# Kernel optimization log

Measured on AMD Instinct MI355X. Metric: run time of the kernel, lower is better.

## Reference

```python
import jax, jax.numpy as jnp
import numpy as np

B, S, D = 2, 1024, 2048
H, KVH, HD = 16, 4, 128
E, K, F = 64, 8, 768
EPS = 1e-6
ROPE_THETA = 1e6


def _rmsnorm(x, w):
    xf = x.astype(jnp.float32)
    n = xf * jax.lax.rsqrt(jnp.mean(xf * xf, axis=-1, keepdims=True) + EPS)
    return n.astype(x.dtype) * w


def _rotate_half(x):
    x1, x2 = jnp.split(x, 2, axis=-1)
    return jnp.concatenate([-x2, x1], axis=-1)


def setup_inputs() -> dict:
    key = jax.random.key(0)
    ks = jax.random.split(key, 12)
    std = 0.02
    x = jax.random.normal(ks[0], (B, S, D), jnp.float32)
    # real RoPE tables (HF style: duplicated half-freqs)
    inv_freq = 1.0 / (ROPE_THETA ** (jnp.arange(0, HD, 2, dtype=jnp.float32) / HD))
    freqs = jnp.arange(S, dtype=jnp.float32)[:, None] * inv_freq[None, :]
    emb = jnp.concatenate([freqs, freqs], axis=-1)  # [S, HD]
    cos = jnp.broadcast_to(jnp.cos(emb)[None], (B, S, HD))
    sin = jnp.broadcast_to(jnp.sin(emb)[None], (B, S, HD))
    return dict(
        x=x, cos=cos, sin=sin,
        ln1_w=jnp.ones((D,), jnp.float32),
        wq=jax.random.normal(ks[1], (D, H * HD), jnp.float32) * std,
        wk=jax.random.normal(ks[2], (D, KVH * HD), jnp.float32) * std,
        wv=jax.random.normal(ks[3], (D, KVH * HD), jnp.float32) * std,
        wo=jax.random.normal(ks[4], (H * HD, D), jnp.float32) * std,
        qn_w=jnp.ones((HD,), jnp.float32),
        kn_w=jnp.ones((HD,), jnp.float32),
        ln2_w=jnp.ones((D,), jnp.float32),
        router_w=jax.random.normal(ks[5], (D, E), jnp.float32) * std,
        w_gate=jax.random.normal(ks[6], (E, D, F), jnp.float32) * std,
        w_up=jax.random.normal(ks[7], (E, D, F), jnp.float32) * std,
        w_down=jax.random.normal(ks[8], (E, F, D), jnp.float32) * std,
    )


def reference(x, cos, sin, ln1_w, wq, wk, wv, wo, qn_w, kn_w, ln2_w,
              router_w, w_gate, w_up, w_down):
    # ---- attention sub-block (pre-norm) ----
    h = _rmsnorm(x, ln1_w)
    q = (h @ wq).reshape(B, S, H, HD)
    k = (h @ wk).reshape(B, S, KVH, HD)
    v = (h @ wv).reshape(B, S, KVH, HD)
    q = _rmsnorm(q, qn_w)  # QK-norm before RoPE
    k = _rmsnorm(k, kn_w)
    q = q.transpose(0, 2, 1, 3)  # [B,H,S,HD]
    k = k.transpose(0, 2, 1, 3)
    v = v.transpose(0, 2, 1, 3)
    c, sn = cos[:, None], sin[:, None]  # [B,1,S,HD]
    q = q * c + _rotate_half(q) * sn
    k = k * c + _rotate_half(k) * sn
    rep = H // KVH
    k = jnp.repeat(k, rep, axis=1)  # GQA repeat_interleave
    v = jnp.repeat(v, rep, axis=1)
    scores = jnp.einsum('bhqd,bhkd->bhqk', q, k) / np.float32(np.sqrt(HD))
    causal = jnp.tril(jnp.ones((S, S), bool))
    scores = jnp.where(causal, scores, jnp.float32(-1e30))
    attn = jax.nn.softmax(scores, axis=-1)
    o = jnp.einsum('bhqk,bhkd->bhqd', attn, v)
    o = o.transpose(0, 2, 1, 3).reshape(B, S, H * HD)
    x = x + o @ wo

    # ---- MoE sub-block (token-choice top-k routing) ----
    T = B * S
    ht = _rmsnorm(x, ln2_w).reshape(T, D)
    logits = ht.astype(jnp.float32) @ router_w
    probs = jax.nn.softmax(logits, axis=-1)  # [T,E]
    topv, topi = jax.lax.top_k(probs, K)
    topv = topv / jnp.sum(topv, axis=-1, keepdims=True)  # norm_topk_prob

    flat_e = topi.reshape(-1)                       # [T*K] expert id per assignment
    flat_t = jnp.repeat(jnp.arange(T), K)           # token id per assignment
    order = jnp.argsort(flat_e)                     # group assignments by expert
    tok = flat_t[order]
    xs = ht[tok]                                    # [T*K, D] dispatched tokens
    group_sizes = jax.ops.segment_sum(
        jnp.ones_like(flat_e, jnp.int32), flat_e, num_segments=E)

    g = jax.lax.ragged_dot(xs, w_gate, group_sizes)         # grouped GEMM
    u = jax.lax.ragged_dot(xs, w_up, group_sizes)
    y = jax.lax.ragged_dot(jax.nn.silu(g) * u, w_down, group_sizes)

    wts = topv.reshape(-1)[order]
    moe = jnp.zeros((T, D), x.dtype).at[tok].add(y * wts[:, None])
    return x + moe.reshape(B, S, D)
```

## Files before the change

### kernel.cpp

```cpp
#include <hip/hip_runtime.h>
#include <math.h>

#define NB     2
#define SEQ    1024
#define TOKS   2048
#define DMODEL 2048
#define NH     16
#define NKV    4
#define HDIM   128
#define NEXP   64
#define TOPK   8
#define FFD    768

__global__ __launch_bounds__(256) void rmsnorm2048_kernel(const float* __restrict__ x,
                                                          const float* __restrict__ w,
                                                          float* __restrict__ out) {
    int t = blockIdx.x;
    const float* xr = x + (size_t)t * DMODEL;
    float* orow = out + (size_t)t * DMODEL;
    int tid = threadIdx.x;
    float4 a = ((const float4*)xr)[tid * 2];
    float4 b = ((const float4*)xr)[tid * 2 + 1];
    float ss = a.x*a.x + a.y*a.y + a.z*a.z + a.w*a.w
             + b.x*b.x + b.y*b.y + b.z*b.z + b.w*b.w;
    __shared__ float red[256];
    red[tid] = ss;
    __syncthreads();
    for (int s = 128; s > 0; s >>= 1) {
        if (tid < s) red[tid] += red[tid + s];
        __syncthreads();
    }
    float rs = rsqrtf(red[0] * (1.0f / DMODEL) + 1e-6f);
    float4 w0 = ((const float4*)w)[tid * 2];
    float4 w1 = ((const float4*)w)[tid * 2 + 1];
    float4 o0, o1;
    o0.x = a.x * rs * w0.x; o0.y = a.y * rs * w0.y; o0.z = a.z * rs * w0.z; o0.w = a.w * rs * w0.w;
    o1.x = b.x * rs * w1.x; o1.y = b.y * rs * w1.y; o1.z = b.z * rs * w1.z; o1.w = b.w * rs * w1.w;
    ((float4*)orow)[tid * 2] = o0;
    ((float4*)orow)[tid * 2 + 1] = o1;
}

__global__ __launch_bounds__(256) void gemm128_kernel(const float* __restrict__ A,
                                                      const float* __restrict__ Bm,
                                                      const float* __restrict__ resid,
                                                      float* __restrict__ C,
                                                      int M, int N, int K) {
    __shared__ float As[16][132];
    __shared__ float Bs[16][132];
    int tid = threadIdx.x;
    int bm = blockIdx.y * 128, bn = blockIdx.x * 128;
    int tx = tid & 15, ty = tid >> 4;
    float acc[8][8];
#pragma unroll
    for (int i = 0; i < 8; ++i)
#pragma unroll
        for (int j = 0; j < 8; ++j) acc[i][j] = 0.f;

    int arow = tid >> 1, acol = (tid & 1) * 8;
    int brow = tid >> 4, bcol = (tid & 15) * 8;
    const float* Aptr = A + (size_t)(bm + arow) * K + acol;
    const float* Bptr = Bm + (size_t)brow * N + bn + bcol;

    for (int k0 = 0; k0 < K; k0 += 16) {
        float4 a0 = *(const float4*)(Aptr + k0);
        float4 a1 = *(const float4*)(Aptr + k0 + 4);
        As[acol + 0][arow] = a0.x; As[acol + 1][arow] = a0.y;
        As[acol + 2][arow] = a0.z; As[acol + 3][arow] = a0.w;
        As[acol + 4][arow] = a1.x; As[acol + 5][arow] = a1.y;
        As[acol + 6][arow] = a1.z; As[acol + 7][arow] = a1.w;
        const float* bp = Bptr + (size_t)k0 * N;
        *(float4*)&Bs[brow][bcol]     = *(const float4*)bp;
        *(float4*)&Bs[brow][bcol + 4] = *(const float4*)(bp + 4);
        __syncthreads();
#pragma unroll
        for (int k = 0; k < 16; ++k) {
            float a[8], b[8];
#pragma unroll
            for (int i = 0; i < 8; ++i) a[i] = As[k][ty * 8 + i];
#pragma unroll
            for (int j = 0; j < 8; ++j) b[j] = Bs[k][tx * 8 + j];
#pragma unroll
            for (int i = 0; i < 8; ++i)
#pragma unroll
                for (int j = 0; j < 8; ++j) acc[i][j] += a[i] * b[j];
        }
        __syncthreads();
    }
#pragma unroll
    for (int i = 0; i < 8; ++i) {
        size_t rowoff = (size_t)(bm + ty * 8 + i) * N + bn + tx * 8;
        float4 c0 = make_float4(acc[i][0], acc[i][1], acc[i][2], acc[i][3]);
        float4 c1 = make_float4(acc[i][4], acc[i][5], acc[i][6], acc[i][7]);
        if (resid) {
            float4 r0 = *(const float4*)(resid + rowoff);
            float4 r1 = *(const float4*)(resid + rowoff + 4);
            c0.x += r0.x; c0.y += r0.y; c0.z += r0.z; c0.w += r0.w;
            c1.x += r1.x; c1.y += r1.y; c1.z += r1.z; c1.w += r1.w;
        }
        *(float4*)(C + rowoff) = c0;
        *(float4*)(C + rowoff + 4) = c1;
    }
}

__global__ __launch_bounds__(128) void qknorm_rope_kernel(float* __restrict__ q, float* __restrict__ kbuf,
                                                          const float* __restrict__ qn_w,
                                                          const float* __restrict__ kn_w,
                                                          const float* __restrict__ cosb,
                                                          const float* __restrict__ sinb) {
    int t = blockIdx.x;
    int head = blockIdx.y;
    int d = threadIdx.x;
    float* buf; const float* w;
    if (head < NH) { buf = q + ((size_t)t * NH + head) * HDIM; w = qn_w; }
    else           { buf = kbuf + ((size_t)t * NKV + (head - NH)) * HDIM; w = kn_w; }
    float v = buf[d];
    __shared__ float red[128];
    __shared__ float nb[128];
    red[d] = v * v;
    __syncthreads();
    for (int s = 64; s > 0; s >>= 1) { if (d < s) red[d] += red[d + s]; __syncthreads(); }
    float rs = rsqrtf(red[0] * (1.0f / HDIM) + 1e-6f);
    float n = v * rs * w[d];
    nb[d] = n;
    __syncthreads();
    float rh = (d < 64) ? -nb[d + 64] : nb[d - 64];
    float c  = cosb[(size_t)t * HDIM + d];
    float s2 = sinb[(size_t)t * HDIM + d];
    buf[d] = n * c + rh * s2;
}

__global__ __launch_bounds__(256) void attn_kernel(const float* __restrict__ q,
                                                   const float* __restrict__ kb,
                                                   const float* __restrict__ vb,
                                                   float* __restrict__ o) {
    int bh = blockIdx.x;
    int b = bh >> 4, hh = bh & 15;
    int kvh = hh >> 2;
    int qt = blockIdx.y;
    int m0 = qt * 32;
    int tid = threadIdx.x;
    __shared__ float Qs[32][132];
    __shared__ float Ks[32][132];
    __shared__ float Vs[32][132];
    __shared__ float Ss[32][33];
    __shared__ float rowm[32], rowl[32], rowa[32];
    const float scale = 0.08838834764831845f;

    int lr = tid >> 3, lc = (tid & 7) * 16;
    {
        const float* src = q + (((size_t)(b * SEQ + m0 + lr)) * NH + hh) * HDIM + lc;
#pragma unroll
        for (int p = 0; p < 4; ++p) {
            float4 v4 = *(const float4*)(src + p * 4);
            Qs[lr][lc + p * 4 + 0] = v4.x * scale;
            Qs[lr][lc + p * 4 + 1] = v4.y * scale;
            Qs[lr][lc + p * 4 + 2] = v4.z * scale;
            Qs[lr][lc + p * 4 + 3] = v4.w * scale;
        }
    }
    if (tid < 32) { rowm[tid] = -1e30f; rowl[tid] = 0.f; }
    float oacc[16];
#pragma unroll
    for (int j = 0; j < 16; ++j) oacc[j] = 0.f;
    int mrow = tid & 31, dbase = (tid >> 5) * 16;
    int mi = tid >> 3, kbase = (tid & 7) * 4;
    __syncthreads();

    for (int kt = 0; kt <= qt; ++kt) {
        int k0 = kt * 32;
        {
            const float* ksrc = kb + (((size_t)(b * SEQ + k0 + lr)) * NKV + kvh) * HDIM + lc;
            const float* vsrc = vb + (((size_t)(b * SEQ + k0 + lr)) * NKV + kvh) * HDIM + lc;
#pragma unroll
            for (int p = 0; p < 4; ++p) {
                *(float4*)&Ks[lr][lc + p * 4] = *(const float4*)(ksrc + p * 4);
                *(float4*)&Vs[lr][lc + p * 4] = *(const float4*)(vsrc + p * 4);
            }
        }
        __syncthreads();
        float sc[4] = {0.f, 0.f, 0.f, 0.f};
#pragma unroll 8
        for (int d4 = 0; d4 < 32; ++d4) {
            float4 qv = *(const float4*)&Qs[mi][d4 * 4];
#pragma unroll
            for (int i = 0; i < 4; ++i) {
                float4 kv = *(const float4*)&Ks[kbase + i][d4 * 4];
                sc[i] += qv.x * kv.x + qv.y * kv.y + qv.z * kv.z + qv.w * kv.w;
            }
        }
#pragma unroll
        for (int i = 0; i < 4; ++i) {
            int kg = k0 + kbase + i;
            Ss[mi][kbase + i] = (kg <= m0 + mi) ? sc[i] : -1e30f;
        }
        __syncthreads();
        if (tid < 32) {
            float mold = rowm[tid];
            float tm = mold;
            for (int j = 0; j < 32; ++j) tm = fmaxf(tm, Ss[tid][j]);
            float al = __expf(mold - tm);
            float sum = 0.f;
            for (int j = 0; j < 32; ++j) {
                float p = __expf(Ss[tid][j] - tm);
                Ss[tid][j] = p;
                sum += p;
            }
            rowa[tid] = al; rowm[tid] = tm;
            rowl[tid] = rowl[tid] * al + sum;
        }
        __syncthreads();
        float al = rowa[mrow];
#pragma unroll
        for (int j = 0; j < 16; ++j) oacc[j] *= al;
        for (int kk = 0; kk < 32; ++kk) {
            float p = Ss[mrow][kk];
            const float* vrow = &Vs[kk][dbase];
#pragma unroll
            for (int j = 0; j < 16; ++j) oacc[j] += p * vrow[j];
        }
        __syncthreads();
    }
    float linv = 1.0f / rowl[mrow];
    float* dst = o + ((size_t)(b * SEQ + m0 + mrow)) * DMODEL + hh * HDIM + dbase;
#pragma unroll
    for (int p = 0; p < 4; ++p) {
        float4 v4 = make_float4(oacc[p * 4 + 0] * linv, oacc[p * 4 + 1] * linv,
                                oacc[p * 4 + 2] * linv, oacc[p * 4 + 3] * linv);
        *(float4*)(dst + p * 4) = v4;
    }
}

__global__ __launch_bounds__(64) void router_kernel(const float* __restrict__ ht,
                                                    const float* __restrict__ rw,
                                                    float* __restrict__ logits) {
    int t = blockIdx.x; int e = threadIdx.x;
    const float* hrow = ht + (size_t)t * DMODEL;
    float acc = 0.f;
    for (int d = 0; d < DMODEL; ++d) acc = fmaf(hrow[d], rw[(size_t)d * NEXP + e], acc);
    logits[(size_t)t * NEXP + e] = acc;
}

__global__ __launch_bounds__(64) void topk_kernel(const float* __restrict__ logits,
                                                  float* __restrict__ topw,
                                                  int* __restrict__ topi) {
    int t = blockIdx.x; int lane = threadIdx.x;
    float v = logits[(size_t)t * NEXP + lane];
    float mx = v;
#pragma unroll
    for (int off = 32; off; off >>= 1) mx = fmaxf(mx, __shfl_xor(mx, off));
    float myv = v;
    float sel_v[TOPK]; int sel_i[TOPK];
#pragma unroll
    for (int it = 0; it < TOPK; ++it) {
        float bv = myv; int bi = lane;
#pragma unroll
        for (int off = 32; off; off >>= 1) {
            float ov = __shfl_xor(bv, off);
            int oi = __shfl_xor(bi, off);
            if (ov > bv || (ov == bv && oi < bi)) { bv = ov; bi = oi; }
        }
        sel_v[it] = bv; sel_i[it] = bi;
        if (lane == bi) myv = -3e38f;
    }
    float sum = 0.f;
#pragma unroll
    for (int it = 0; it < TOPK; ++it) sum += __expf(sel_v[it] - mx);
    if (lane == 0) {
#pragma unroll
        for (int it = 0; it < TOPK; ++it) {
            topw[(size_t)t * TOPK + it] = __expf(sel_v[it] - mx) / sum;
            topi[(size_t)t * TOPK + it] = sel_i[it];
        }
    }
}

__global__ void zero_small_kernel(int* cnt, int* pos) {
    int i = threadIdx.x;
    if (i < NEXP) { cnt[i] = 0; pos[i] = 0; }
}
__global__ void hist_kernel(const int* __restrict__ topi, int* __restrict__ cnt) {
    int i = blockIdx.x * 256 + threadIdx.x;
    if (i < TOKS * TOPK) atomicAdd(&cnt[topi[i]], 1);
}
__global__ void scan_kernel(const int* __restrict__ cnt, int* __restrict__ eoff) {
    if (threadIdx.x == 0) {
        int a = 0;
        for (int e = 0; e < NEXP; ++e) { eoff[e] = a; a += cnt[e]; }
    }
}
__global__ void scatter_kernel(const int* __restrict__ topi, const float* __restrict__ topw,
                               const int* __restrict__ eoff, int* __restrict__ pos,
                               int* __restrict__ tokl, float* __restrict__ wtl) {
    int i = blockIdx.x * 256 + threadIdx.x;
    if (i >= TOKS * TOPK) return;
    int e = topi[i];
    int slot = atomicAdd(&pos[e], 1);
    int idx = eoff[e] + slot;
    tokl[idx] = i >> 3;
    wtl[idx] = topw[i];
}

__global__ __launch_bounds__(256) void moe_gateup_kernel(const float* __restrict__ ht,
                                                         const float* __restrict__ wg,
                                                         const float* __restrict__ wu,
                                                         const int* __restrict__ tokl,
                                                         const float* __restrict__ wtl,
                                                         const int* __restrict__ eoff,
                                                         const int* __restrict__ ecnt,
                                                         float* __restrict__ act) {
    int e = blockIdx.x, ft = blockIdx.y, mt = blockIdx.z;
    int ne = ecnt[e];
    int r0 = mt * 64;
    if (r0 >= ne) return;
    int base = eoff[e];
    int tid = threadIdx.x;
    __shared__ float As[16][68];
    __shared__ float Gs[16][64];
    __shared__ float Us[16][64];
    int arow = tid >> 2, acol = (tid & 3) * 4;
    int grow = r0 + arow;
    const float* asrc = (grow < ne) ? (ht + (size_t)tokl[base + grow] * DMODEL) : nullptr;
    int wrow = tid >> 4, wcol = (tid & 15) * 4;
    const float* wgp = wg + (size_t)e * DMODEL * FFD + (size_t)ft * 64;
    const float* wup = wu + (size_t)e * DMODEL * FFD + (size_t)ft * 64;
    int tx = tid & 15, ty = tid >> 4;
    float aG[4][4], aU[4][4];
#pragma unroll
    for (int i = 0; i < 4; ++i)
#pragma unroll
        for (int j = 0; j < 4; ++j) { aG[i][j] = 0.f; aU[i][j] = 0.f; }

    for (int k0 = 0; k0 < DMODEL; k0 += 16) {
        float4 av = asrc ? *(const float4*)(asrc + k0 + acol) : make_float4(0.f, 0.f, 0.f, 0.f);
        As[acol + 0][arow] = av.x; As[acol + 1][arow] = av.y;
        As[acol + 2][arow] = av.z; As[acol + 3][arow] = av.w;
        *(float4*)&Gs[wrow][wcol] = *(const float4*)(wgp + (size_t)(k0 + wrow) * FFD + wcol);
        *(float4*)&Us[wrow][wcol] = *(const float4*)(wup + (size_t)(k0 + wrow) * FFD + wcol);
        __syncthreads();
#pragma unroll
        for (int k = 0; k < 16; ++k) {
            float a[4], g[4], u[4];
#pragma unroll
            for (int i = 0; i < 4; ++i) a[i] = As[k][ty * 4 + i];
#pragma unroll
            for (int j = 0; j < 4; ++j) { g[j] = Gs[k][tx * 4 + j]; u[j] = Us[k][tx * 4 + j]; }
#pragma unroll
            for (int i = 0; i < 4; ++i)
#pragma unroll
                for (int j = 0; j < 4; ++j) {
                    aG[i][j] += a[i] * g[j];
                    aU[i][j] += a[i] * u[j];
                }
        }
        __syncthreads();
    }
#pragma unroll
    for (int i = 0; i < 4; ++i) {
        int gr = r0 + ty * 4 + i;
        if (gr < ne) {
            float wt = wtl[base + gr];
            float* dst = act + (size_t)(base + gr) * FFD + ft * 64 + tx * 4;
#pragma unroll
            for (int j = 0; j < 4; ++j) {
                float g = aG[i][j];
                float sg = g / (1.f + __expf(-g));
                dst[j] = sg * aU[i][j] * wt;
            }
        }
    }
}

__global__ __launch_bounds__(256) void moe_down_kernel(const float* __restrict__ act,
                                                       const float* __restrict__ wd,
                                                       const int* __restrict__ tokl,
                                                       const int* __restrict__ eoff,
                                                       const int* __restrict__ ecnt,
                                                       float* __restrict__ out) {
    int e = blockIdx.x, dt = blockIdx.y, mt = blockIdx.z;
    int ne = ecnt[e];
    int r0 = mt * 64;
    if (r0 >= ne) return;
    int base = eoff[e];
    int tid = threadIdx.x;
    __shared__ float As[16][68];
    __shared__ float Ws[16][64];
    int arow = tid >> 2, acol = (tid & 3) * 4;
    int grow = r0 + arow;
    const float* asrc = (grow < ne) ? (act + (size_t)(base + grow) * FFD) : nullptr;
    int wrow = tid >> 4, wcol = (tid & 15) * 4;
    const float* wdp = wd + (size_t)e * FFD * DMODEL + (size_t)dt * 64;
    int tx = tid & 15, ty = tid >> 4;
    float acc[4][4];
#pragma unroll
    for (int i = 0; i < 4; ++i)
#pragma unroll
        for (int j = 0; j < 4; ++j) acc[i][j] = 0.f;

    for (int k0 = 0; k0 < FFD; k0 += 16) {
        float4 av = asrc ? *(const float4*)(asrc + k0 + acol) : make_float4(0.f, 0.f, 0.f, 0.f);
        As[acol + 0][arow] = av.x; As[acol + 1][arow] = av.y;
        As[acol + 2][arow] = av.z; As[acol + 3][arow] = av.w;
        *(float4*)&Ws[wrow][wcol] = *(const float4*)(wdp + (size_t)(k0 + wrow) * DMODEL + wcol);
        __syncthreads();
#pragma unroll
        for (int k = 0; k < 16; ++k) {
            float a[4], b[4];
#pragma unroll
            for (int i = 0; i < 4; ++i) a[i] = As[k][ty * 4 + i];
#pragma unroll
            for (int j = 0; j < 4; ++j) b[j] = Ws[k][tx * 4 + j];
#pragma unroll
            for (int i = 0; i < 4; ++i)
#pragma unroll
                for (int j = 0; j < 4; ++j) acc[i][j] += a[i] * b[j];
        }
        __syncthreads();
    }
#pragma unroll
    for (int i = 0; i < 4; ++i) {
        int gr = r0 + ty * 4 + i;
        if (gr < ne) {
            int tok = tokl[base + gr];
            float* dst = out + (size_t)tok * DMODEL + dt * 64 + tx * 4;
#pragma unroll
            for (int j = 0; j < 4; ++j) atomicAdd(dst + j, acc[i][j]);
        }
    }
}

extern "C" void kernel_launch(void* const* d_in, const int* in_sizes, int n_in,
                              void* d_out, int out_size, void* d_ws, size_t ws_size,
                              hipStream_t stream) {
    const float* x    = (const float*)d_in[0];
    const float* cosb = (const float*)d_in[1];
    const float* sinb = (const float*)d_in[2];
    const float* ln1  = (const float*)d_in[3];
    const float* wq   = (const float*)d_in[4];
    const float* wk   = (const float*)d_in[5];
    const float* wv   = (const float*)d_in[6];
    const float* wo   = (const float*)d_in[7];
    const float* qnw  = (const float*)d_in[8];
    const float* knw  = (const float*)d_in[9];
    const float* ln2  = (const float*)d_in[10];
    const float* rw   = (const float*)d_in[11];
    const float* wg   = (const float*)d_in[12];
    const float* wu   = (const float*)d_in[13];
    const float* wd   = (const float*)d_in[14];
    float* out = (float*)d_out;

    float* ws     = (float*)d_ws;
    float* h      = ws;
    float* qb     = h + 4194304;
    float* kbuf   = qb + 4194304;
    float* vbuf   = kbuf + 1048576;
    float* act    = vbuf + 1048576;
    float* logits = act + 12582912;
    float* topw   = logits + 131072;
    float* wtl    = topw + 16384;
    int* topi     = (int*)(wtl + 16384);
    int* tokl     = topi + 16384;
    int* cnt      = tokl + 16384;
    int* eoff     = cnt + 64;
    int* pos      = eoff + 64;
    float* attn_o = h;
    float* ht     = qb;

    rmsnorm2048_kernel<<<TOKS, 256, 0, stream>>>(x, ln1, h);
    gemm128_kernel<<<dim3(16, 16), 256, 0, stream>>>(h, wq, nullptr, qb, TOKS, 2048, DMODEL);
    gemm128_kernel<<<dim3(4, 16), 256, 0, stream>>>(h, wk, nullptr, kbuf, TOKS, 512, DMODEL);
    gemm128_kernel<<<dim3(4, 16), 256, 0, stream>>>(h, wv, nullptr, vbuf, TOKS, 512, DMODEL);
    qknorm_rope_kernel<<<dim3(TOKS, NH + NKV), 128, 0, stream>>>(qb, kbuf, qnw, knw, cosb, sinb);
    attn_kernel<<<dim3(NB * NH, SEQ / 32), 256, 0, stream>>>(qb, kbuf, vbuf, attn_o);
    gemm128_kernel<<<dim3(16, 16), 256, 0, stream>>>(attn_o, wo, x, out, TOKS, 2048, DMODEL);
    rmsnorm2048_kernel<<<TOKS, 256, 0, stream>>>(out, ln2, ht);
    router_kernel<<<TOKS, 64, 0, stream>>>(ht, rw, logits);
    topk_kernel<<<TOKS, 64, 0, stream>>>(logits, topw, topi);
    zero_small_kernel<<<1, 64, 0, stream>>>(cnt, pos);
    hist_kernel<<<64, 256, 0, stream>>>(topi, cnt);
    scan_kernel<<<1, 1, 0, stream>>>(cnt, eoff);
    scatter_kernel<<<64, 256, 0, stream>>>(topi, topw, eoff, pos, tokl, wtl);
    moe_gateup_kernel<<<dim3(NEXP, FFD / 64, 32), 256, 0, stream>>>(ht, wg, wu, tokl, wtl, eoff, cnt, act);
    moe_down_kernel<<<dim3(NEXP, DMODEL / 64, 32), 256, 0, stream>>>(act, wd, tokl, eoff, cnt, out);
}
```

Before: 5.000 ms.

## Use split-bf16 MFMA for MoE grouped GEMMs with precomputed hi/lo activations

Replaces the scalar FP32 MoE gate/up and down GEMMs with MFMA bf16 kernels. Each operand is split into bf16 hi and lo parts and multiplied with three MFMAs to approximate FP32 accuracy. The second rmsnorm now also writes bf16 hi/lo copies of the normalized activations, and the gate/up kernel stores the activation as hi/lo bf16. Weights are still read as fp32 and split on the fly, using an XOR-swizzled LDS layout. The grid order is changed so that tiles of the same expert are adjacent. The cost is extra conversion work and a small loss of precision from dropping the lo*lo term.

```diff
diff --git a/kernel.cpp b/kernel.cpp
--- a/kernel.cpp
+++ b/kernel.cpp
@@ -12,9 +12,24 @@
 #define TOPK   8
 #define FFD    768
 
+typedef __attribute__((ext_vector_type(8))) short bf16x8;
+typedef __attribute__((ext_vector_type(4))) float f32x4;
+
+__device__ __forceinline__ void split2(float a, float b, unsigned int& hp, unsigned int& lp) {
+    unsigned int h, l;
+    asm("v_cvt_pk_bf16_f32 %0, %1, %2" : "=v"(h) : "v"(a), "v"(b));
+    float hf0 = __uint_as_float(h << 16);
+    float hf1 = __uint_as_float(h & 0xffff0000u);
+    float l0 = a - hf0, l1 = b - hf1;
+    asm("v_cvt_pk_bf16_f32 %0, %1, %2" : "=v"(l) : "v"(l0), "v"(l1));
+    hp = h; lp = l;
+}
+
 __global__ __launch_bounds__(256) void rmsnorm2048_kernel(const float* __restrict__ x,
                                                           const float* __restrict__ w,
-                                                          float* __restrict__ out) {
+                                                          float* __restrict__ out,
+                                                          unsigned short* __restrict__ hi,
+                                                          unsigned short* __restrict__ lo) {
     int t = blockIdx.x;
     const float* xr = x + (size_t)t * DMODEL;
     float* orow = out + (size_t)t * DMODEL;
@@ -38,6 +53,16 @@
     o1.x = b.x * rs * w1.x; o1.y = b.y * rs * w1.y; o1.z = b.z * rs * w1.z; o1.w = b.w * rs * w1.w;
     ((float4*)orow)[tid * 2] = o0;
     ((float4*)orow)[tid * 2 + 1] = o1;
+    if (hi) {
+        unsigned int h0, l0_, h1, l1_, h2, l2_, h3, l3_;
+        split2(o0.x, o0.y, h0, l0_);
+        split2(o0.z, o0.w, h1, l1_);
+        split2(o1.x, o1.y, h2, l2_);
+        split2(o1.z, o1.w, h3, l3_);
+        size_t off = (size_t)t * DMODEL + (size_t)tid * 8;
+        *(uint4*)(hi + off) = make_uint4(h0, h1, h2, h3);
+        *(uint4*)(lo + off) = make_uint4(l0_, l1_, l2_, l3_);
+    }
 }
 
 __global__ __launch_bounds__(256) void gemm128_kernel(const float* __restrict__ A,
@@ -300,132 +325,228 @@
     wtl[idx] = topw[i];
 }
 
-__global__ __launch_bounds__(256) void moe_gateup_kernel(const float* __restrict__ ht,
-                                                         const float* __restrict__ wg,
-                                                         const float* __restrict__ wu,
-                                                         const int* __restrict__ tokl,
-                                                         const float* __restrict__ wtl,
-                                                         const int* __restrict__ eoff,
-                                                         const int* __restrict__ ecnt,
-                                                         float* __restrict__ act) {
-    int e = blockIdx.x, ft = blockIdx.y, mt = blockIdx.z;
+#define LROW 40
+__device__ __forceinline__ int lds_off(int row, int kc) {
+    return row * LROW + (((kc ^ (row >> 3)) & 3) << 3);
+}
+
+__global__ __launch_bounds__(256) void moe_gateup_mfma(
+        const unsigned short* __restrict__ hthi, const unsigned short* __restrict__ htlo,
+        const float* __restrict__ wg, const float* __restrict__ wu,
+        const int* __restrict__ tokl, const float* __restrict__ wtl,
+        const int* __restrict__ eoff, const int* __restrict__ ecnt,
+        unsigned short* __restrict__ acthi, unsigned short* __restrict__ actlo) {
+    int mt = blockIdx.x, ft = blockIdx.y, e = blockIdx.z;
     int ne = ecnt[e];
     int r0 = mt * 64;
     if (r0 >= ne) return;
     int base = eoff[e];
     int tid = threadIdx.x;
-    __shared__ float As[16][68];
-    __shared__ float Gs[16][64];
-    __shared__ float Us[16][64];
-    int arow = tid >> 2, acol = (tid & 3) * 4;
-    int grow = r0 + arow;
-    const float* asrc = (grow < ne) ? (ht + (size_t)tokl[base + grow] * DMODEL) : nullptr;
-    int wrow = tid >> 4, wcol = (tid & 15) * 4;
-    const float* wgp = wg + (size_t)e * DMODEL * FFD + (size_t)ft * 64;
-    const float* wup = wu + (size_t)e * DMODEL * FFD + (size_t)ft * 64;
-    int tx = tid & 15, ty = tid >> 4;
-    float aG[4][4], aU[4][4];
-#pragma unroll
-    for (int i = 0; i < 4; ++i)
-#pragma unroll
-        for (int j = 0; j < 4; ++j) { aG[i][j] = 0.f; aU[i][j] = 0.f; }
-
-    for (int k0 = 0; k0 < DMODEL; k0 += 16) {
-        float4 av = asrc ? *(const float4*)(asrc + k0 + acol) : make_float4(0.f, 0.f, 0.f, 0.f);
-        As[acol + 0][arow] = av.x; As[acol + 1][arow] = av.y;
-        As[acol + 2][arow] = av.z; As[acol + 3][arow] = av.w;
-        *(float4*)&Gs[wrow][wcol] = *(const float4*)(wgp + (size_t)(k0 + wrow) * FFD + wcol);
-        *(float4*)&Us[wrow][wcol] = *(const float4*)(wup + (size_t)(k0 + wrow) * FFD + wcol);
-        __syncthreads();
-#pragma unroll
-        for (int k = 0; k < 16; ++k) {
-            float a[4], g[4], u[4];
-#pragma unroll
-            for (int i = 0; i < 4; ++i) a[i] = As[k][ty * 4 + i];
-#pragma unroll
-            for (int j = 0; j < 4; ++j) { g[j] = Gs[k][tx * 4 + j]; u[j] = Us[k][tx * 4 + j]; }
-#pragma unroll
-            for (int i = 0; i < 4; ++i)
-#pragma unroll
-                for (int j = 0; j < 4; ++j) {
-                    aG[i][j] += a[i] * g[j];
-                    aU[i][j] += a[i] * u[j];
-                }
-        }
-        __syncthreads();
-    }
-#pragma unroll
-    for (int i = 0; i < 4; ++i) {
-        int gr = r0 + ty * 4 + i;
-        if (gr < ne) {
-            float wt = wtl[base + gr];
-            float* dst = act + (size_t)(base + gr) * FFD + ft * 64 + tx * 4;
-#pragma unroll
-            for (int j = 0; j < 4; ++j) {
-                float g = aG[i][j];
-                float sg = g / (1.f + __expf(-g));
-                dst[j] = sg * aU[i][j] * wt;
+
+    __shared__ __align__(16) unsigned short Ah[64 * LROW], Al[64 * LROW];
+    __shared__ __align__(16) unsigned short Gh[64 * LROW], Gl[64 * LROW];
+    __shared__ __align__(16) unsigned short Uh[64 * LROW], Ul[64 * LROW];
+
+    int arow = tid >> 2, akc = tid & 3;
+    const unsigned short* ahsrc = nullptr;
+    const unsigned short* alsrc = nullptr;
+    if (r0 + arow < ne) {
+        size_t o = (size_t)tokl[base + r0 + arow] * DMODEL + akc * 8;
+        ahsrc = hthi + o;
+        alsrc = htlo + o;
+    }
+    int bn = tid & 63, bkc = tid >> 6;
+    const float* wgp = wg + (size_t)e * DMODEL * FFD + (size_t)ft * 64 + bn;
+    const float* wup = wu + (size_t)e * DMODEL * FFD + (size_t)ft * 64 + bn;
+
+    int lane = tid & 63, wave = tid >> 6;
+    int wr = wave >> 1, wc = wave & 1;
+    int lrow = lane & 15, lkc = lane >> 4;
+
+    f32x4 z4 = {0.f, 0.f, 0.f, 0.f};
+    f32x4 accG[2][2], accU[2][2];
+#pragma unroll
+    for (int m = 0; m < 2; ++m)
+#pragma unroll
+        for (int n = 0; n < 2; ++n) { accG[m][n] = z4; accU[m][n] = z4; }
+
+    int aoff[2], boff[2];
+#pragma unroll
+    for (int m = 0; m < 2; ++m) aoff[m] = lds_off(wr * 32 + m * 16 + lrow, lkc);
+#pragma unroll
+    for (int n = 0; n < 2; ++n) boff[n] = lds_off(wc * 32 + n * 16 + lrow, lkc);
+    int awoff = lds_off(arow, akc);
+    int bwoff = lds_off(bn, bkc);
+
+    const bf16x8 zero8 = {0, 0, 0, 0, 0, 0, 0, 0};
+
+    for (int k0 = 0; k0 < DMODEL; k0 += 32) {
+        bf16x8 avh = ahsrc ? *(const bf16x8*)(ahsrc + k0) : zero8;
+        bf16x8 avl = alsrc ? *(const bf16x8*)(alsrc + k0) : zero8;
+        float gv[8], uv[8];
+#pragma unroll
+        for (int j = 0; j < 8; ++j) {
+            size_t ro = (size_t)(k0 + bkc * 8 + j) * FFD;
+            gv[j] = wgp[ro];
+            uv[j] = wup[ro];
+        }
+        unsigned int ghp[4], glp[4], uhp[4], ulp[4];
+#pragma unroll
+        for (int p = 0; p < 4; ++p) {
+            split2(gv[2 * p], gv[2 * p + 1], ghp[p], glp[p]);
+            split2(uv[2 * p], uv[2 * p + 1], uhp[p], ulp[p]);
+        }
+        __syncthreads();
+        *(bf16x8*)(Ah + awoff) = avh;
+        *(bf16x8*)(Al + awoff) = avl;
+        *(uint4*)(Gh + bwoff) = make_uint4(ghp[0], ghp[1], ghp[2], ghp[3]);
+        *(uint4*)(Gl + bwoff) = make_uint4(glp[0], glp[1], glp[2], glp[3]);
+        *(uint4*)(Uh + bwoff) = make_uint4(uhp[0], uhp[1], uhp[2], uhp[3]);
+        *(uint4*)(Ul + bwoff) = make_uint4(ulp[0], ulp[1], ulp[2], ulp[3]);
+        __syncthreads();
+
+        bf16x8 a_h[2], a_l[2];
+#pragma unroll
+        for (int m = 0; m < 2; ++m) {
+            a_h[m] = *(const bf16x8*)(Ah + aoff[m]);
+            a_l[m] = *(const bf16x8*)(Al + aoff[m]);
+        }
+#pragma unroll
+        for (int n = 0; n < 2; ++n) {
+            bf16x8 g_h = *(const bf16x8*)(Gh + boff[n]);
+            bf16x8 g_l = *(const bf16x8*)(Gl + boff[n]);
+            bf16x8 u_h = *(const bf16x8*)(Uh + boff[n]);
+            bf16x8 u_l = *(const bf16x8*)(Ul + boff[n]);
+#pragma unroll
+            for (int m = 0; m < 2; ++m) {
+                accG[m][n] = __builtin_amdgcn_mfma_f32_16x16x32_bf16(a_h[m], g_h, accG[m][n], 0, 0, 0);
+                accG[m][n] = __builtin_amdgcn_mfma_f32_16x16x32_bf16(a_l[m], g_h, accG[m][n], 0, 0, 0);
+                accG[m][n] = __builtin_amdgcn_mfma_f32_16x16x32_bf16(a_h[m], g_l, accG[m][n], 0, 0, 0);
+                accU[m][n] = __builtin_amdgcn_mfma_f32_16x16x32_bf16(a_h[m], u_h, accU[m][n], 0, 0, 0);
+                accU[m][n] = __builtin_amdgcn_mfma_f32_16x16x32_bf16(a_l[m], u_h, accU[m][n], 0, 0, 0);
+                accU[m][n] = __builtin_amdgcn_mfma_f32_16x16x32_bf16(a_h[m], u_l, accU[m][n], 0, 0, 0);
             }
         }
     }
-}
-
-__global__ __launch_bounds__(256) void moe_down_kernel(const float* __restrict__ act,
-                                                       const float* __restrict__ wd,
-                                                       const int* __restrict__ tokl,
-                                                       const int* __restrict__ eoff,
-                                                       const int* __restrict__ ecnt,
-                                                       float* __restrict__ out) {
-    int e = blockIdx.x, dt = blockIdx.y, mt = blockIdx.z;
+
+    int crow4 = (lane >> 4) * 4;
+#pragma unroll
+    for (int m = 0; m < 2; ++m)
+#pragma unroll
+        for (int r = 0; r < 4; ++r) {
+            int gr = r0 + wr * 32 + m * 16 + crow4 + r;
+            if (gr < ne) {
+                float wt = wtl[base + gr];
+                size_t rowoff = (size_t)(base + gr) * FFD + ft * 64 + wc * 32 + lrow;
+                float g0 = accG[m][0][r], g1 = accG[m][1][r];
+                float u0 = accU[m][0][r], u1 = accU[m][1][r];
+                float x0 = g0 / (1.f + __expf(-g0)) * u0 * wt;
+                float x1 = g1 / (1.f + __expf(-g1)) * u1 * wt;
+                unsigned int hp, lp;
+                split2(x0, x1, hp, lp);
+                acthi[rowoff]      = (unsigned short)(hp & 0xffffu);
+                acthi[rowoff + 16] = (unsigned short)(hp >> 16);
+                actlo[rowoff]      = (unsigned short)(lp & 0xffffu);
+                actlo[rowoff + 16] = (unsigned short)(lp >> 16);
+            }
+        }
+}
+
+__global__ __launch_bounds__(256) void moe_down_mfma(
+        const unsigned short* __restrict__ acthi, const unsigned short* __restrict__ actlo,
+        const float* __restrict__ wd,
+        const int* __restrict__ tokl, const int* __restrict__ eoff, const int* __restrict__ ecnt,
+        float* __restrict__ out) {
+    int mt = blockIdx.x, dt = blockIdx.y, e = blockIdx.z;
     int ne = ecnt[e];
     int r0 = mt * 64;
     if (r0 >= ne) return;
     int base = eoff[e];
     int tid = threadIdx.x;
-    __shared__ float As[16][68];
-    __shared__ float Ws[16][64];
-    int arow = tid >> 2, acol = (tid & 3) * 4;
-    int grow = r0 + arow;
-    const float* asrc = (grow < ne) ? (act + (size_t)(base + grow) * FFD) : nullptr;
-    int wrow = tid >> 4, wcol = (tid & 15) * 4;
-    const float* wdp = wd + (size_t)e * FFD * DMODEL + (size_t)dt * 64;
-    int tx = tid & 15, ty = tid >> 4;
-    float acc[4][4];
-#pragma unroll
-    for (int i = 0; i < 4; ++i)
-#pragma unroll
-        for (int j = 0; j < 4; ++j) acc[i][j] = 0.f;
-
-    for (int k0 = 0; k0 < FFD; k0 += 16) {
-        float4 av = asrc ? *(const float4*)(asrc + k0 + acol) : make_float4(0.f, 0.f, 0.f, 0.f);
-        As[acol + 0][arow] = av.x; As[acol + 1][arow] = av.y;
-        As[acol + 2][arow] = av.z; As[acol + 3][arow] = av.w;
-        *(float4*)&Ws[wrow][wcol] = *(const float4*)(wdp + (size_t)(k0 + wrow) * DMODEL + wcol);
-        __syncthreads();
-#pragma unroll
-        for (int k = 0; k < 16; ++k) {
-            float a[4], b[4];
-#pragma unroll
-            for (int i = 0; i < 4; ++i) a[i] = As[k][ty * 4 + i];
-#pragma unroll
-            for (int j = 0; j < 4; ++j) b[j] = Ws[k][tx * 4 + j];
-#pragma unroll
-            for (int i = 0; i < 4; ++i)
-#pragma unroll
-                for (int j = 0; j < 4; ++j) acc[i][j] += a[i] * b[j];
-        }
-        __syncthreads();
-    }
-#pragma unroll
-    for (int i = 0; i < 4; ++i) {
-        int gr = r0 + ty * 4 + i;
-        if (gr < ne) {
-            int tok = tokl[base + gr];
-            float* dst = out + (size_t)tok * DMODEL + dt * 64 + tx * 4;
-#pragma unroll
-            for (int j = 0; j < 4; ++j) atomicAdd(dst + j, acc[i][j]);
-        }
-    }
+
+    __shared__ __align__(16) unsigned short Ah[64 * LROW], Al[64 * LROW];
+    __shared__ __align__(16) unsigned short Wh[64 * LROW], Wl[64 * LROW];
+
+    int arow = tid >> 2, akc = tid & 3;
+    const unsigned short* ahsrc = nullptr;
+    const unsigned short* alsrc = nullptr;
+    if (r0 + arow < ne) {
+        size_t o = (size_t)(base + r0 + arow) * FFD + akc * 8;
+        ahsrc = acthi + o;
+        alsrc = actlo + o;
+    }
+    int bn = tid & 63, bkc = tid >> 6;
+    const float* wdp = wd + (size_t)e * FFD * DMODEL + (size_t)dt * 64 + bn;
+
+    int lane = tid & 63, wave = tid >> 6;
+    int wr = wave >> 1, wc = wave & 1;
+    int lrow = lane & 15, lkc = lane >> 4;
+
+    f32x4 z4 = {0.f, 0.f, 0.f, 0.f};
+    f32x4 acc[2][2];
+#pragma unroll
+    for (int m = 0; m < 2; ++m)
+#pragma unroll
+        for (int n = 0; n < 2; ++n) acc[m][n] = z4;
+
+    int aoff[2], boff[2];
+#pragma unroll
+    for (int m = 0; m < 2; ++m) aoff[m] = lds_off(wr * 32 + m * 16 + lrow, lkc);
+#pragma unroll
+    for (int n = 0; n < 2; ++n) boff[n] = lds_off(wc * 32 + n * 16 + lrow, lkc);
+    int awoff = lds_off(arow, akc);
+    int bwoff = lds_off(bn, bkc);
+
+    const bf16x8 zero8 = {0, 0, 0, 0, 0, 0, 0, 0};
+
+    for (int k0 = 0; k0 < FFD; k0 += 32) {
+        bf16x8 avh = ahsrc ? *(const bf16x8*)(ahsrc + k0) : zero8;
+        bf16x8 avl = alsrc ? *(const bf16x8*)(alsrc + k0) : zero8;
+        float wv[8];
+#pragma unroll
+        for (int j = 0; j < 8; ++j) wv[j] = wdp[(size_t)(k0 + bkc * 8 + j) * DMODEL];
+        unsigned int whp[4], wlp[4];
+#pragma unroll
+        for (int p = 0; p < 4; ++p) split2(wv[2 * p], wv[2 * p + 1], whp[p], wlp[p]);
+        __syncthreads();
+        *(bf16x8*)(Ah + awoff) = avh;
+        *(bf16x8*)(Al + awoff) = avl;
+        *(uint4*)(Wh + bwoff) = make_uint4(whp[0], whp[1], whp[2], whp[3]);
+        *(uint4*)(Wl + bwoff) = make_uint4(wlp[0], wlp[1], wlp[2], wlp[3]);
+        __syncthreads();
+
+        bf16x8 a_h[2], a_l[2];
+#pragma unroll
+        for (int m = 0; m < 2; ++m) {
+            a_h[m] = *(const bf16x8*)(Ah + aoff[m]);
+            a_l[m] = *(const bf16x8*)(Al + aoff[m]);
+        }
+#pragma unroll
+        for (int n = 0; n < 2; ++n) {
+            bf16x8 w_h = *(const bf16x8*)(Wh + boff[n]);
+            bf16x8 w_l = *(const bf16x8*)(Wl + boff[n]);
+#pragma unroll
+            for (int m = 0; m < 2; ++m) {
+                acc[m][n] = __builtin_amdgcn_mfma_f32_16x16x32_bf16(a_h[m], w_h, acc[m][n], 0, 0, 0);
+                acc[m][n] = __builtin_amdgcn_mfma_f32_16x16x32_bf16(a_l[m], w_h, acc[m][n], 0, 0, 0);
+                acc[m][n] = __builtin_amdgcn_mfma_f32_16x16x32_bf16(a_h[m], w_l, acc[m][n], 0, 0, 0);
+            }
+        }
+    }
+
+    int crow4 = (lane >> 4) * 4;
+#pragma unroll
+    for (int m = 0; m < 2; ++m)
+#pragma unroll
+        for (int r = 0; r < 4; ++r) {
+            int gr = r0 + wr * 32 + m * 16 + crow4 + r;
+            if (gr < ne) {
+                int tok = tokl[base + gr];
+                float* dst = out + (size_t)tok * DMODEL + dt * 64 + wc * 32 + lrow;
+                atomicAdd(dst, acc[m][0][r]);
+                atomicAdd(dst + 16, acc[m][1][r]);
+            }
+        }
 }
 
 extern "C" void kernel_launch(void* const* d_in, const int* in_sizes, int n_in,
@@ -465,20 +586,25 @@
     float* attn_o = h;
     float* ht     = qb;
 
-    rmsnorm2048_kernel<<<TOKS, 256, 0, stream>>>(x, ln1, h);
+    unsigned short* acthi = (unsigned short*)act;
+    unsigned short* actlo = acthi + (size_t)16384 * FFD;
+    unsigned short* hthi  = (unsigned short*)h;
+    unsigned short* htlo  = hthi + (size_t)TOKS * DMODEL;
+
+    rmsnorm2048_kernel<<<TOKS, 256, 0, stream>>>(x, ln1, h, nullptr, nullptr);
     gemm128_kernel<<<dim3(16, 16), 256, 0, stream>>>(h, wq, nullptr, qb, TOKS, 2048, DMODEL);
     gemm128_kernel<<<dim3(4, 16), 256, 0, stream>>>(h, wk, nullptr, kbuf, TOKS, 512, DMODEL);
     gemm128_kernel<<<dim3(4, 16), 256, 0, stream>>>(h, wv, nullptr, vbuf, TOKS, 512, DMODEL);
     qknorm_rope_kernel<<<dim3(TOKS, NH + NKV), 128, 0, stream>>>(qb, kbuf, qnw, knw, cosb, sinb);
     attn_kernel<<<dim3(NB * NH, SEQ / 32), 256, 0, stream>>>(qb, kbuf, vbuf, attn_o);
     gemm128_kernel<<<dim3(16, 16), 256, 0, stream>>>(attn_o, wo, x, out, TOKS, 2048, DMODEL);
-    rmsnorm2048_kernel<<<TOKS, 256, 0, stream>>>(out, ln2, ht);
+    rmsnorm2048_kernel<<<TOKS, 256, 0, stream>>>(out, ln2, ht, hthi, htlo);
     router_kernel<<<TOKS, 64, 0, stream>>>(ht, rw, logits);
     topk_kernel<<<TOKS, 64, 0, stream>>>(logits, topw, topi);
     zero_small_kernel<<<1, 64, 0, stream>>>(cnt, pos);
     hist_kernel<<<64, 256, 0, stream>>>(topi, cnt);
     scan_kernel<<<1, 1, 0, stream>>>(cnt, eoff);
     scatter_kernel<<<64, 256, 0, stream>>>(topi, topw, eoff, pos, tokl, wtl);
-    moe_gateup_kernel<<<dim3(NEXP, FFD / 64, 32), 256, 0, stream>>>(ht, wg, wu, tokl, wtl, eoff, cnt, act);
-    moe_down_kernel<<<dim3(NEXP, DMODEL / 64, 32), 256, 0, stream>>>(act, wd, tokl, eoff, cnt, out);
-}
+    moe_gateup_mfma<<<dim3(32, FFD / 64, NEXP), 256, 0, stream>>>(hthi, htlo, wg, wu, tokl, wtl, eoff, cnt, acthi, actlo);
+    moe_down_mfma<<<dim3(32, DMODEL / 64, NEXP), 256, 0, stream>>>(acthi, actlo, wd, tokl, eoff, cnt, out);
+}
```

Measured after the change: 7.376 ms. +47.5%, slower.
